# Optimization experiments

Measured on AMD Instinct MI355X. Metric: run time of the kernel, lower is better.

## Reference

```python
import jax, jax.numpy as jnp
import numpy as np

IOU_THRESH = 0.6
IMG_SIZE = 2048.0


def _iou_matrix(boxes):
    # boxes: [N, 4] as (x1, y1, x2, y2)
    x1, y1, x2, y2 = boxes[:, 0], boxes[:, 1], boxes[:, 2], boxes[:, 3]
    area = jnp.maximum(x2 - x1, 0.0) * jnp.maximum(y2 - y1, 0.0)  # [N]
    ix1 = jnp.maximum(x1[:, None], x1[None, :])
    iy1 = jnp.maximum(y1[:, None], y1[None, :])
    ix2 = jnp.minimum(x2[:, None], x2[None, :])
    iy2 = jnp.minimum(y2[:, None], y2[None, :])
    inter = jnp.maximum(ix2 - ix1, 0.0) * jnp.maximum(iy2 - iy1, 0.0)  # [N, N]
    union = area[:, None] + area[None, :] - inter
    return inter / jnp.maximum(union, 1e-9)


def _nms_keep(boxes, thresh):
    # Greedy NMS in the given (score-sorted) order; returns a [N] bool keep mask.
    n = boxes.shape[0]
    iou = _iou_matrix(boxes)  # [N, N] -- dominant memory traffic
    idx = jnp.arange(n)

    def step(suppressed, i):
        keep_i = jnp.logical_not(suppressed[i])
        # a kept box suppresses all LATER boxes with IoU > thresh
        suppressed = suppressed | (keep_i & (idx > i) & (iou[i] > thresh))
        return suppressed, keep_i

    _, keep = jax.lax.scan(step, jnp.zeros((n,), dtype=bool), idx)
    return keep


def _make_boxes(kc, ks, n):
    c = jax.random.uniform(kc, (n, 2), minval=0.0, maxval=IMG_SIZE)
    s = jax.random.uniform(ks, (n, 2), minval=10.0, maxval=120.0)
    return jnp.concatenate([c - s / 2, c + s / 2], axis=1)  # [n, 4]


def setup_inputs() -> dict:
    key = jax.random.key(0)
    k1, k2, k3, k4, k5, k6 = jax.random.split(key, 6)
    N = 8192  # vstacked detections across projections
    M = 8192  # vstacked RPN rois across projections
    det_boxes = _make_boxes(k1, k2, N)
    cls_scores = jax.random.normal(k3, (N, 4), dtype=jnp.float32)  # 4 TL classes, class 0 = invalid
    proj_id = jnp.zeros((N, 1), dtype=jnp.float32)
    detections = jnp.concatenate([proj_id, det_boxes, cls_scores], axis=1)  # [N, 9]
    rpn_boxes = _make_boxes(k4, k5, M)
    objness = jax.random.uniform(k6, (M, 1), dtype=jnp.float32)
    rpn_data = jnp.concatenate([jnp.zeros((M, 1), dtype=jnp.float32), rpn_boxes, objness], axis=1)  # [M, 6]
    return {"detections": detections, "rpn_data": rpn_data}


def reference(detections, rpn_data):
    # detect(): NMS(0.6) on detections[:, 1:5] and on rpn_data[:, 1:5]
    keep_det = _nms_keep(detections[:, 1:5], IOU_THRESH)  # [N] bool
    keep_rpn = _nms_keep(rpn_data[:, 1:5], IOU_THRESH)    # [M] bool
    # forward(): split surviving detections into valid (tl_type != 0) / invalid
    tl_types = jnp.argmax(detections[:, 5:], axis=1)
    valid_mask = keep_det & (tl_types != 0)
    invalid_mask = keep_det & (tl_types == 0)
    # fixed-shape (jit-friendly) masked outputs instead of data-dependent gather
    valid_detections = detections * valid_mask[:, None].astype(detections.dtype)
    invalid_detections = detections * invalid_mask[:, None].astype(detections.dtype)
    rpn_attack_data = rpn_data * keep_rpn[:, None].astype(rpn_data.dtype)
    return valid_detections, invalid_detections, rpn_attack_data
```

## Files before the change

kernel.cpp:

```cpp
#include <hip/hip_runtime.h>


constexpr int NROWS = 8192;
constexpr int NKW   = 256;
constexpr unsigned ACAP = 512;
constexpr unsigned BCAP = 1536;
constexpr unsigned RCAP = 2048;
constexpr unsigned ELDS = 16384;
#define IOU_T 0.6f

constexpr size_t OFF_ECNT  = 0;
constexpr size_t OFF_BCNT  = 2048;
constexpr size_t OFF_OVF   = 4096;
constexpr size_t OFF_EDGES = 8192;
constexpr size_t OFF_BBOX  = OFF_EDGES + (size_t)512 * RCAP * 4;
constexpr size_t OFF_BID   = OFF_BBOX  + (size_t)512 * ACAP * 16;

__global__ __launch_bounds__(512) void bin_kernel(
    const float* __restrict__ det, const float* __restrict__ rpn,
    unsigned* __restrict__ binCnt, float4* __restrict__ binBox,
    unsigned* __restrict__ binId, unsigned* __restrict__ ovf)
{
  const int b = blockIdx.x;
  const int set = b >> 4;
  const int r = ((b & 15) << 9) + threadIdx.x;
  const float* src  = (set == 0) ? det : rpn;
  const int    strd = (set == 0) ? 9 : 6;

  const float* p = src + (size_t)r * strd + 1;
  const float x1 = p[0], y1 = p[1], x2 = p[2], y2 = p[3];
  const float cxe = 0.5f * (x1 + x2), cye = 0.5f * (y1 + y2);
  const int ccx = min(15, max(0, (int)(cxe * (1.0f / 128.0f))));
  const int ccy = min(15, max(0, (int)(cye * (1.0f / 128.0f))));
  const unsigned cell = (unsigned)(set * 256 + ccy * 16 + ccx);

  const unsigned slot = atomicAdd(&binCnt[cell], 1u);
  if (slot < ACAP) {
    binBox[(size_t)cell * ACAP + slot] = make_float4(x1, y1, x2, y2);
    binId [(size_t)cell * ACAP + slot] = (unsigned)r;
  } else {
    atomicOr(ovf, 1u);
  }
}

__global__ __launch_bounds__(512) void pair_kernel(
    const float* __restrict__ det, const float* __restrict__ rpn,
    const unsigned* __restrict__ binCnt, const float4* __restrict__ binBox,
    const unsigned* __restrict__ binId, const unsigned* __restrict__ ovfp,
    unsigned* __restrict__ cnts, unsigned* __restrict__ edges)
{
  const int cellid = blockIdx.x, set = blockIdx.y;
  const int cx = cellid & 15, cy = cellid >> 4;
  unsigned* myedges = edges + ((size_t)(set * 256 + cellid)) * RCAP;

  __shared__ float4 B4[BCAP];
  __shared__ float  Bar[BCAP];
  __shared__ unsigned Bid[BCAP];
  __shared__ unsigned ncell[9], ncnt[9], noff[9];
  __shared__ unsigned nN_sh, na_sh, nb_sh, eCnt, bad;

  const int t = threadIdx.x;
  if (t == 0) {
    unsigned nN = 0;
    ncell[nN++] = (unsigned)(set * 256 + cellid);
    for (int dy = -1; dy <= 1; ++dy)
      for (int dx = -1; dx <= 1; ++dx) {
        if (dx == 0 && dy == 0) continue;
        const int nx = cx + dx, ny = cy + dy;
        if (nx >= 0 && nx < 16 && ny >= 0 && ny < 16)
          ncell[nN++] = (unsigned)(set * 256 + ny * 16 + nx);
      }
    nN_sh = nN; eCnt = 0u; bad = *ovfp;
  }
  __syncthreads();
  const unsigned nN = nN_sh;
  if (t < (int)nN) ncnt[t] = min(binCnt[ncell[t]], ACAP);
  __syncthreads();
  if (t == 0) {
    unsigned off = 0;
    for (unsigned n = 0; n < nN; ++n) { noff[n] = off; off += ncnt[n]; }
    na_sh = ncnt[0]; nb_sh = off;
    if (off > BCAP) bad = 1u;
  }
  __syncthreads();

  const unsigned na = na_sh, nb = nb_sh;
  const bool ok = (bad == 0u);

  if (ok) {
    for (unsigned idx = t; idx < nb; idx += 512) {
      unsigned n = 0;
      while (idx >= noff[n] + ncnt[n]) ++n;
      const unsigned k = idx - noff[n];
      const size_t  g = (size_t)ncell[n] * ACAP + k;
      const float4 bx = binBox[g];
      B4[idx]  = bx;
      Bar[idx] = fmaxf(bx.z - bx.x, 0.0f) * fmaxf(bx.w - bx.y, 0.0f);
      Bid[idx] = binId[g];
    }
  }
  __syncthreads();

  if (ok) {
    const unsigned tot = na * nb;
    for (unsigned p = t; p < tot; p += 512) {
      const unsigned ai = p / nb, x = p - ai * nb;
      const unsigned ia = Bid[ai], ib = Bid[x];
      if (ia < ib) {
        const float4 A = B4[ai], B = B4[x];
        const float ix1 = fmaxf(A.x, B.x), iy1 = fmaxf(A.y, B.y);
        const float ix2 = fminf(A.z, B.z), iy2 = fminf(A.w, B.w);
        const float inter = fmaxf(ix2 - ix1, 0.0f) * fmaxf(iy2 - iy1, 0.0f);
        if (inter > 0.0f) {
          const float uni = Bar[ai] + Bar[x] - inter;
          const float iou = inter / fmaxf(uni, 1e-9f);
          if (iou > IOU_T) {
            const unsigned slot = atomicAdd(&eCnt, 1u);
            if (slot < RCAP) myedges[slot] = (ia << 13) | ib;
          }
        }
      }
    }
  } else {
    const float* src  = (set == 0) ? det : rpn;
    const int    strd = (set == 0) ? 9 : 6;
    for (int ra = 0; ra < NROWS; ++ra) {
      const float* pa = src + (size_t)ra * strd + 1;
      const float ax1 = pa[0], ay1 = pa[1], ax2 = pa[2], ay2 = pa[3];
      const float cxe = 0.5f * (ax1 + ax2), cye = 0.5f * (ay1 + ay2);
      const int ccx = min(15, max(0, (int)(cxe * (1.0f / 128.0f))));
      const int ccy = min(15, max(0, (int)(cye * (1.0f / 128.0f))));
      if (ccx != cx || ccy != cy) continue;
      const float aar = fmaxf(ax2 - ax1, 0.0f) * fmaxf(ay2 - ay1, 0.0f);
      for (int rb = t; rb < NROWS; rb += 512) {
        if ((unsigned)ra >= (unsigned)rb) continue;
        const float* pb = src + (size_t)rb * strd + 1;
        const float bx1 = pb[0], by1 = pb[1], bx2 = pb[2], by2 = pb[3];
        const float ix1 = fmaxf(ax1, bx1), iy1 = fmaxf(ay1, by1);
        const float ix2 = fminf(ax2, bx2), iy2 = fminf(ay2, by2);
        const float inter = fmaxf(ix2 - ix1, 0.0f) * fmaxf(iy2 - iy1, 0.0f);
        if (inter > 0.0f) {
          const float bar = fmaxf(bx2 - bx1, 0.0f) * fmaxf(by2 - by1, 0.0f);
          const float uni = aar + bar - inter;
          const float iou = inter / fmaxf(uni, 1e-9f);
          if (iou > IOU_T) {
            const unsigned slot = atomicAdd(&eCnt, 1u);
            if (slot < RCAP) myedges[slot] = ((unsigned)ra << 13) | (unsigned)rb;
          }
        }
      }
    }
  }
  __syncthreads();
  if (t == 0) cnts[set * 256 + cellid] = min(eCnt, RCAP);
}

__global__ __launch_bounds__(1024) void solve_epi_kernel(
    const float* __restrict__ det, const float* __restrict__ rpn,
    const unsigned* __restrict__ cnts, const unsigned* __restrict__ edges,
    float* __restrict__ out)
{
  const int blk = blockIdx.x;
  const int set = blk >> 4;
  const int slice = blk & 15;
  const unsigned* gedges = edges + (size_t)set * 256 * RCAP;

  __shared__ unsigned eL[ELDS];
  __shared__ unsigned rcnt[256], roff[256];
  __shared__ unsigned kbuf[2][NKW];
  __shared__ int changed[2];
  __shared__ unsigned Etot_sh;
  __shared__ float vmsk[512], imsk[512];

  const int t = threadIdx.x;
  if (t < 256) rcnt[t] = min(cnts[set * 256 + t], RCAP);
  __syncthreads();

  if (t < 64) {
    const unsigned h0 = rcnt[4 * t], h1 = rcnt[4 * t + 1];
    const unsigned h2 = rcnt[4 * t + 2], h3 = rcnt[4 * t + 3];
    const unsigned lsum = h0 + h1 + h2 + h3;
    unsigned incl = lsum;
    #pragma unroll
    for (int d = 1; d < 64; d <<= 1) {
      const unsigned v = __shfl_up(incl, d);
      if (t >= d) incl += v;
    }
    const unsigned base = incl - lsum;
    roff[4 * t] = base;               roff[4 * t + 1] = base + h0;
    roff[4 * t + 2] = base + h0 + h1; roff[4 * t + 3] = base + h0 + h1 + h2;
    if (t == 63) Etot_sh = incl;
  }
  if (t < NKW) kbuf[0][t] = 0xFFFFFFFFu;
  __syncthreads();

  const unsigned Etot = Etot_sh;
  const bool cached = (Etot <= ELDS);
  if (cached) {
    const unsigned rg = (unsigned)t >> 2, ln = (unsigned)t & 3u;
    const unsigned c = rcnt[rg], o = roff[rg];
    for (unsigned k = ln; k < c; k += 4u)
      eL[o + k] = gedges[(size_t)rg * RCAP + k];
  }
  __syncthreads();

  int cur = 0;
  for (int round = 0; round < NROWS + 8; ++round) {
    const int nxt = cur ^ 1;
    if (t == 0) changed[round & 1] = 0;
    if (t < NKW) kbuf[nxt][t] = 0xFFFFFFFFu;
    __syncthreads();

    if (cached) {
      for (unsigned e = t; e < Etot; e += 1024) {
        const unsigned pk = eL[e];
        const unsigned i = pk >> 13, j = pk & 8191u;
        if ((kbuf[cur][i >> 5] >> (i & 31)) & 1u)
          atomicAnd(&kbuf[nxt][j >> 5], ~(1u << (j & 31)));
      }
    } else {
      for (unsigned r = (unsigned)t >> 2; r < 256u; r += 256u) {
        const unsigned c = rcnt[r];
        for (unsigned k = (unsigned)t & 3u; k < c; k += 4u) {
          const unsigned pk = gedges[(size_t)r * RCAP + k];
          const unsigned i = pk >> 13, j = pk & 8191u;
          if ((kbuf[cur][i >> 5] >> (i & 31)) & 1u)
            atomicAnd(&kbuf[nxt][j >> 5], ~(1u << (j & 31)));
        }
      }
    }
    __syncthreads();

    if (t < NKW && kbuf[nxt][t] != kbuf[cur][t]) changed[round & 1] = 1;
    __syncthreads();

    cur = nxt;
    if (!changed[round & 1]) break;
  }

  const int r0 = slice * 512;
  if (set == 0) {
    if (t < 512) {
      const int i = r0 + t;
      const bool kd = (kbuf[cur][i >> 5] >> (i & 31)) & 1u;
      const float* p = det + (size_t)i * 9;
      const float sc0 = p[5], sc1 = p[6], sc2 = p[7], sc3 = p[8];
      int am = 0; float best = sc0;
      if (sc1 > best) { best = sc1; am = 1; }
      if (sc2 > best) { best = sc2; am = 2; }
      if (sc3 > best) { best = sc3; am = 3; }
      vmsk[t] = (kd && am != 0) ? 1.0f : 0.0f;
      imsk[t] = (kd && am == 0) ? 1.0f : 0.0f;
    }
    __syncthreads();
    const float4* in4 = reinterpret_cast<const float4*>(det + (size_t)r0 * 9);
    float4* o0 = reinterpret_cast<float4*>(out + (size_t)r0 * 9);
    float4* o1 = reinterpret_cast<float4*>(out + (size_t)NROWS * 9 + (size_t)r0 * 9);
    for (int q = t; q < 1152; q += 1024) {
      const float4 v = in4[q];
      const float* vp = reinterpret_cast<const float*>(&v);
      float4 a, b;
      float* ap = reinterpret_cast<float*>(&a);
      float* bp = reinterpret_cast<float*>(&b);
      #pragma unroll
      for (int j = 0; j < 4; ++j) {
        const unsigned d = (unsigned)(q * 4 + j);
        const unsigned row = (d * 7282u) >> 16;
        ap[j] = vp[j] * vmsk[row];
        bp[j] = vp[j] * imsk[row];
      }
      o0[q] = a; o1[q] = b;
    }
  } else {
    if (t < 512) {
      const int i = r0 + t;
      const bool kr = (kbuf[cur][i >> 5] >> (i & 31)) & 1u;
      vmsk[t] = kr ? 1.0f : 0.0f;
    }
    __syncthreads();
    const float4* in4 = reinterpret_cast<const float4*>(rpn + (size_t)r0 * 6);
    float4* o2 = reinterpret_cast<float4*>(out + (size_t)NROWS * 18 + (size_t)r0 * 6);
    for (int q = t; q < 768; q += 1024) {
      const float4 v = in4[q];
      const float* vp = reinterpret_cast<const float*>(&v);
      float4 a;
      float* ap = reinterpret_cast<float*>(&a);
      #pragma unroll
      for (int j = 0; j < 4; ++j) {
        const unsigned d = (unsigned)(q * 4 + j);
        const unsigned row = (d * 10923u) >> 16;
        ap[j] = vp[j] * vmsk[row];
      }
      o2[q] = a;
    }
  }
}

extern "C" void kernel_launch(void* const* d_in, const int* in_sizes, int n_in,
                              void* d_out, int out_size, void* d_ws, size_t ws_size,
                              hipStream_t stream)
{
  const float* det = (const float*)d_in[0];
  const float* rpn = (const float*)d_in[1];
  float* out = (float*)d_out;

  char* ws = (char*)d_ws;
  unsigned* ecnt   = (unsigned*)(ws + OFF_ECNT);
  unsigned* binCnt = (unsigned*)(ws + OFF_BCNT);
  unsigned* ovf    = (unsigned*)(ws + OFF_OVF);
  unsigned* edges  = (unsigned*)(ws + OFF_EDGES);
  float4*   binBox = (float4*)  (ws + OFF_BBOX);
  unsigned* binId  = (unsigned*)(ws + OFF_BID);

  hipMemsetAsync(ws + OFF_BCNT, 0, 2048 + 64, stream);

  bin_kernel<<<32, 512, 0, stream>>>(det, rpn, binCnt, binBox, binId, ovf);

  dim3 g1(256, 2);
  pair_kernel<<<g1, 512, 0, stream>>>(det, rpn, binCnt, binBox, binId, ovf,
                                      ecnt, edges);

  solve_epi_kernel<<<32, 1024, 0, stream>>>(det, rpn, ecnt, edges, out);
}
```

Baseline: 79.49 us.

## Fuse bin, pair and solve stages into one cooperative kernel with grid syncs

Replaces the memset and three separate kernel launches with a single cooperative kernel of 512 blocks that zeroes the counters, bins boxes, builds IoU edges per cell and runs the iterative NMS solve, separated by grid.sync() barriers. Shared memory for the pair and solve phases is overlaid through a union. The solve phase drops from 1024 to 512 threads per block, and the LDS edge cache shrinks from 16384 to 12288 entries to fit the tighter occupancy target. The aim is to remove launch and memset overhead. In exchange it pays grid-barrier costs, leaves only 32 blocks active during the long solve loop, gives that loop half the threads, and falls back to global edge reads more often because the cache is smaller.

```diff
diff --git a/kernel.cpp b/kernel.cpp
--- a/kernel.cpp
+++ b/kernel.cpp
@@ -1,4 +1,7 @@
 #include <hip/hip_runtime.h>
+#include <hip/hip_cooperative_groups.h>
+
+namespace cg = cooperative_groups;
 
 
 constexpr int NROWS = 8192;
@@ -6,7 +9,7 @@
 constexpr unsigned ACAP = 512;
 constexpr unsigned BCAP = 1536;
 constexpr unsigned RCAP = 2048;
-constexpr unsigned ELDS = 16384;
+constexpr unsigned ELDS = 12288;
 #define IOU_T 0.6f
 
 constexpr size_t OFF_ECNT  = 0;
@@ -16,169 +19,178 @@
 constexpr size_t OFF_BBOX  = OFF_EDGES + (size_t)512 * RCAP * 4;
 constexpr size_t OFF_BID   = OFF_BBOX  + (size_t)512 * ACAP * 16;
 
-__global__ __launch_bounds__(512) void bin_kernel(
+union __align__(16) Smem {
+  struct {
+    float4   B4[BCAP];
+    float    Bar[BCAP];
+    unsigned Bid[BCAP];
+  } p;
+  struct {
+    unsigned eL[ELDS];
+    unsigned rcnt[256], roff[256];
+    unsigned kbuf[2][NKW];
+    float    vmsk[512], imsk[512];
+  } s;
+};
+
+__global__ __launch_bounds__(512, 4) void fused_kernel(
     const float* __restrict__ det, const float* __restrict__ rpn,
-    unsigned* __restrict__ binCnt, float4* __restrict__ binBox,
-    unsigned* __restrict__ binId, unsigned* __restrict__ ovf)
+    unsigned* __restrict__ ecnt, unsigned* __restrict__ binCnt,
+    unsigned* __restrict__ ovf,  unsigned* __restrict__ edges,
+    float4* __restrict__ binBox, unsigned* __restrict__ binId,
+    float* __restrict__ out)
 {
-  const int b = blockIdx.x;
-  const int set = b >> 4;
-  const int r = ((b & 15) << 9) + threadIdx.x;
-  const float* src  = (set == 0) ? det : rpn;
-  const int    strd = (set == 0) ? 9 : 6;
-
-  const float* p = src + (size_t)r * strd + 1;
-  const float x1 = p[0], y1 = p[1], x2 = p[2], y2 = p[3];
-  const float cxe = 0.5f * (x1 + x2), cye = 0.5f * (y1 + y2);
-  const int ccx = min(15, max(0, (int)(cxe * (1.0f / 128.0f))));
-  const int ccy = min(15, max(0, (int)(cye * (1.0f / 128.0f))));
-  const unsigned cell = (unsigned)(set * 256 + ccy * 16 + ccx);
-
-  const unsigned slot = atomicAdd(&binCnt[cell], 1u);
-  if (slot < ACAP) {
-    binBox[(size_t)cell * ACAP + slot] = make_float4(x1, y1, x2, y2);
-    binId [(size_t)cell * ACAP + slot] = (unsigned)r;
-  } else {
-    atomicOr(ovf, 1u);
-  }
-}
-
-__global__ __launch_bounds__(512) void pair_kernel(
-    const float* __restrict__ det, const float* __restrict__ rpn,
-    const unsigned* __restrict__ binCnt, const float4* __restrict__ binBox,
-    const unsigned* __restrict__ binId, const unsigned* __restrict__ ovfp,
-    unsigned* __restrict__ cnts, unsigned* __restrict__ edges)
-{
-  const int cellid = blockIdx.x, set = blockIdx.y;
-  const int cx = cellid & 15, cy = cellid >> 4;
-  unsigned* myedges = edges + ((size_t)(set * 256 + cellid)) * RCAP;
-
-  __shared__ float4 B4[BCAP];
-  __shared__ float  Bar[BCAP];
-  __shared__ unsigned Bid[BCAP];
-  __shared__ unsigned ncell[9], ncnt[9], noff[9];
-  __shared__ unsigned nN_sh, na_sh, nb_sh, eCnt, bad;
-
-  const int t = threadIdx.x;
-  if (t == 0) {
-    unsigned nN = 0;
-    ncell[nN++] = (unsigned)(set * 256 + cellid);
-    for (int dy = -1; dy <= 1; ++dy)
-      for (int dx = -1; dx <= 1; ++dx) {
-        if (dx == 0 && dy == 0) continue;
-        const int nx = cx + dx, ny = cy + dy;
-        if (nx >= 0 && nx < 16 && ny >= 0 && ny < 16)
-          ncell[nN++] = (unsigned)(set * 256 + ny * 16 + nx);
-      }
-    nN_sh = nN; eCnt = 0u; bad = *ovfp;
-  }
-  __syncthreads();
-  const unsigned nN = nN_sh;
-  if (t < (int)nN) ncnt[t] = min(binCnt[ncell[t]], ACAP);
-  __syncthreads();
-  if (t == 0) {
-    unsigned off = 0;
-    for (unsigned n = 0; n < nN; ++n) { noff[n] = off; off += ncnt[n]; }
-    na_sh = ncnt[0]; nb_sh = off;
-    if (off > BCAP) bad = 1u;
-  }
-  __syncthreads();
-
-  const unsigned na = na_sh, nb = nb_sh;
-  const bool ok = (bad == 0u);
-
-  if (ok) {
-    for (unsigned idx = t; idx < nb; idx += 512) {
-      unsigned n = 0;
-      while (idx >= noff[n] + ncnt[n]) ++n;
-      const unsigned k = idx - noff[n];
-      const size_t  g = (size_t)ncell[n] * ACAP + k;
-      const float4 bx = binBox[g];
-      B4[idx]  = bx;
-      Bar[idx] = fmaxf(bx.z - bx.x, 0.0f) * fmaxf(bx.w - bx.y, 0.0f);
-      Bid[idx] = binId[g];
-    }
-  }
-  __syncthreads();
-
-  if (ok) {
-    const unsigned tot = na * nb;
-    for (unsigned p = t; p < tot; p += 512) {
-      const unsigned ai = p / nb, x = p - ai * nb;
-      const unsigned ia = Bid[ai], ib = Bid[x];
-      if (ia < ib) {
-        const float4 A = B4[ai], B = B4[x];
-        const float ix1 = fmaxf(A.x, B.x), iy1 = fmaxf(A.y, B.y);
-        const float ix2 = fminf(A.z, B.z), iy2 = fminf(A.w, B.w);
-        const float inter = fmaxf(ix2 - ix1, 0.0f) * fmaxf(iy2 - iy1, 0.0f);
-        if (inter > 0.0f) {
-          const float uni = Bar[ai] + Bar[x] - inter;
-          const float iou = inter / fmaxf(uni, 1e-9f);
-          if (iou > IOU_T) {
-            const unsigned slot = atomicAdd(&eCnt, 1u);
-            if (slot < RCAP) myedges[slot] = (ia << 13) | ib;
+  cg::grid_group grid = cg::this_grid();
+  __shared__ Smem U;
+  __shared__ unsigned ncell[9], ncnt9[9], noff9[9];
+  __shared__ unsigned nN_sh, na_sh, nb_sh, eC, bad;
+  __shared__ unsigned Etot_sh;
+  __shared__ int changed[2];
+
+  const int bid = blockIdx.x;
+  const int t   = threadIdx.x;
+
+  if (bid == 0) { binCnt[t] = 0u; if (t == 0) *ovf = 0u; }
+  grid.sync();
+
+  {
+    const int gtid = (bid << 9) + t;
+    if (gtid < 2 * NROWS) {
+      const int bset = gtid >> 13;
+      const int r    = gtid & (NROWS - 1);
+      const float* src  = (bset == 0) ? det : rpn;
+      const int    strd = (bset == 0) ? 9 : 6;
+      const float* p = src + (size_t)r * strd + 1;
+      const float x1 = p[0], y1 = p[1], x2 = p[2], y2 = p[3];
+      const float cxe = 0.5f * (x1 + x2), cye = 0.5f * (y1 + y2);
+      const int ccx = min(15, max(0, (int)(cxe * (1.0f / 128.0f))));
+      const int ccy = min(15, max(0, (int)(cye * (1.0f / 128.0f))));
+      const unsigned cell = (unsigned)(bset * 256 + ccy * 16 + ccx);
+      const unsigned slot = atomicAdd(&binCnt[cell], 1u);
+      if (slot < ACAP) {
+        binBox[(size_t)cell * ACAP + slot] = make_float4(x1, y1, x2, y2);
+        binId [(size_t)cell * ACAP + slot] = (unsigned)r;
+      } else {
+        atomicOr(ovf, 1u);
+      }
+    }
+  }
+  grid.sync();
+
+  {
+    const int set = bid >> 8;
+    const int cellid = bid & 255;
+    const int cx = cellid & 15, cy = cellid >> 4;
+    unsigned* myedges = edges + ((size_t)(set * 256 + cellid)) * RCAP;
+
+    if (t == 0) {
+      unsigned nN = 0;
+      ncell[nN++] = (unsigned)(set * 256 + cellid);
+      for (int dy = -1; dy <= 1; ++dy)
+        for (int dx = -1; dx <= 1; ++dx) {
+          if (dx == 0 && dy == 0) continue;
+          const int nx = cx + dx, ny = cy + dy;
+          if (nx >= 0 && nx < 16 && ny >= 0 && ny < 16)
+            ncell[nN++] = (unsigned)(set * 256 + ny * 16 + nx);
+        }
+      nN_sh = nN; eC = 0u; bad = *ovf;
+    }
+    __syncthreads();
+    const unsigned nN = nN_sh;
+    if (t < (int)nN) ncnt9[t] = min(binCnt[ncell[t]], ACAP);
+    __syncthreads();
+    if (t == 0) {
+      unsigned off = 0;
+      for (unsigned n = 0; n < nN; ++n) { noff9[n] = off; off += ncnt9[n]; }
+      na_sh = ncnt9[0]; nb_sh = off;
+      if (off > BCAP) bad = 1u;
+    }
+    __syncthreads();
+
+    const unsigned na = na_sh, nb = nb_sh;
+    const bool ok = (bad == 0u);
+
+    if (ok) {
+      for (unsigned idx = t; idx < nb; idx += 512) {
+        unsigned n = 0;
+        while (idx >= noff9[n] + ncnt9[n]) ++n;
+        const unsigned k = idx - noff9[n];
+        const size_t  g = (size_t)ncell[n] * ACAP + k;
+        const float4 bx = binBox[g];
+        U.p.B4[idx]  = bx;
+        U.p.Bar[idx] = fmaxf(bx.z - bx.x, 0.0f) * fmaxf(bx.w - bx.y, 0.0f);
+        U.p.Bid[idx] = binId[g];
+      }
+    }
+    __syncthreads();
+
+    if (ok) {
+      const unsigned tot = na * nb;
+      for (unsigned pi = t; pi < tot; pi += 512) {
+        const unsigned ai = pi / nb, x = pi - ai * nb;
+        const unsigned ia = U.p.Bid[ai], ib = U.p.Bid[x];
+        if (ia < ib) {
+          const float4 A = U.p.B4[ai], B = U.p.B4[x];
+          const float ix1 = fmaxf(A.x, B.x), iy1 = fmaxf(A.y, B.y);
+          const float ix2 = fminf(A.z, B.z), iy2 = fminf(A.w, B.w);
+          const float inter = fmaxf(ix2 - ix1, 0.0f) * fmaxf(iy2 - iy1, 0.0f);
+          if (inter > 0.0f) {
+            const float uni = U.p.Bar[ai] + U.p.Bar[x] - inter;
+            const float iou = inter / fmaxf(uni, 1e-9f);
+            if (iou > IOU_T) {
+              const unsigned slot = atomicAdd(&eC, 1u);
+              if (slot < RCAP) myedges[slot] = (ia << 13) | ib;
+            }
           }
         }
       }
-    }
-  } else {
-    const float* src  = (set == 0) ? det : rpn;
-    const int    strd = (set == 0) ? 9 : 6;
-    for (int ra = 0; ra < NROWS; ++ra) {
-      const float* pa = src + (size_t)ra * strd + 1;
-      const float ax1 = pa[0], ay1 = pa[1], ax2 = pa[2], ay2 = pa[3];
-      const float cxe = 0.5f * (ax1 + ax2), cye = 0.5f * (ay1 + ay2);
-      const int ccx = min(15, max(0, (int)(cxe * (1.0f / 128.0f))));
-      const int ccy = min(15, max(0, (int)(cye * (1.0f / 128.0f))));
-      if (ccx != cx || ccy != cy) continue;
-      const float aar = fmaxf(ax2 - ax1, 0.0f) * fmaxf(ay2 - ay1, 0.0f);
-      for (int rb = t; rb < NROWS; rb += 512) {
-        if ((unsigned)ra >= (unsigned)rb) continue;
-        const float* pb = src + (size_t)rb * strd + 1;
-        const float bx1 = pb[0], by1 = pb[1], bx2 = pb[2], by2 = pb[3];
-        const float ix1 = fmaxf(ax1, bx1), iy1 = fmaxf(ay1, by1);
-        const float ix2 = fminf(ax2, bx2), iy2 = fminf(ay2, by2);
-        const float inter = fmaxf(ix2 - ix1, 0.0f) * fmaxf(iy2 - iy1, 0.0f);
-        if (inter > 0.0f) {
-          const float bar = fmaxf(bx2 - bx1, 0.0f) * fmaxf(by2 - by1, 0.0f);
-          const float uni = aar + bar - inter;
-          const float iou = inter / fmaxf(uni, 1e-9f);
-          if (iou > IOU_T) {
-            const unsigned slot = atomicAdd(&eCnt, 1u);
-            if (slot < RCAP) myedges[slot] = ((unsigned)ra << 13) | (unsigned)rb;
+    } else {
+      const float* src  = (set == 0) ? det : rpn;
+      const int    strd = (set == 0) ? 9 : 6;
+      for (int ra = 0; ra < NROWS; ++ra) {
+        const float* pa = src + (size_t)ra * strd + 1;
+        const float ax1 = pa[0], ay1 = pa[1], ax2 = pa[2], ay2 = pa[3];
+        const float cxe = 0.5f * (ax1 + ax2), cye = 0.5f * (ay1 + ay2);
+        const int ccx = min(15, max(0, (int)(cxe * (1.0f / 128.0f))));
+        const int ccy = min(15, max(0, (int)(cye * (1.0f / 128.0f))));
+        if (ccx != cx || ccy != cy) continue;
+        const float aar = fmaxf(ax2 - ax1, 0.0f) * fmaxf(ay2 - ay1, 0.0f);
+        for (int rb = t; rb < NROWS; rb += 512) {
+          if ((unsigned)ra >= (unsigned)rb) continue;
+          const float* pb = src + (size_t)rb * strd + 1;
+          const float bx1 = pb[0], by1 = pb[1], bx2 = pb[2], by2 = pb[3];
+          const float ix1 = fmaxf(ax1, bx1), iy1 = fmaxf(ay1, by1);
+          const float ix2 = fminf(ax2, bx2), iy2 = fminf(ay2, by2);
+          const float inter = fmaxf(ix2 - ix1, 0.0f) * fmaxf(iy2 - iy1, 0.0f);
+          if (inter > 0.0f) {
+            const float bar = fmaxf(bx2 - bx1, 0.0f) * fmaxf(by2 - by1, 0.0f);
+            const float uni = aar + bar - inter;
+            const float iou = inter / fmaxf(uni, 1e-9f);
+            if (iou > IOU_T) {
+              const unsigned slot = atomicAdd(&eC, 1u);
+              if (slot < RCAP) myedges[slot] = ((unsigned)ra << 13) | (unsigned)rb;
+            }
           }
         }
       }
     }
-  }
+    __syncthreads();
+    if (t == 0) ecnt[set * 256 + cellid] = min(eC, RCAP);
+  }
+  grid.sync();
+
+  if (bid >= 32) return;
+
+  const int set = bid >> 4;
+  const int slice = bid & 15;
+  const unsigned* gedges = edges + (size_t)set * 256 * RCAP;
+
+  if (t < 256) U.s.rcnt[t] = min(ecnt[set * 256 + t], RCAP);
   __syncthreads();
-  if (t == 0) cnts[set * 256 + cellid] = min(eCnt, RCAP);
-}
-
-__global__ __launch_bounds__(1024) void solve_epi_kernel(
-    const float* __restrict__ det, const float* __restrict__ rpn,
-    const unsigned* __restrict__ cnts, const unsigned* __restrict__ edges,
-    float* __restrict__ out)
-{
-  const int blk = blockIdx.x;
-  const int set = blk >> 4;
-  const int slice = blk & 15;
-  const unsigned* gedges = edges + (size_t)set * 256 * RCAP;
-
-  __shared__ unsigned eL[ELDS];
-  __shared__ unsigned rcnt[256], roff[256];
-  __shared__ unsigned kbuf[2][NKW];
-  __shared__ int changed[2];
-  __shared__ unsigned Etot_sh;
-  __shared__ float vmsk[512], imsk[512];
-
-  const int t = threadIdx.x;
-  if (t < 256) rcnt[t] = min(cnts[set * 256 + t], RCAP);
-  __syncthreads();
 
   if (t < 64) {
-    const unsigned h0 = rcnt[4 * t], h1 = rcnt[4 * t + 1];
-    const unsigned h2 = rcnt[4 * t + 2], h3 = rcnt[4 * t + 3];
+    const unsigned h0 = U.s.rcnt[4 * t], h1 = U.s.rcnt[4 * t + 1];
+    const unsigned h2 = U.s.rcnt[4 * t + 2], h3 = U.s.rcnt[4 * t + 3];
     const unsigned lsum = h0 + h1 + h2 + h3;
     unsigned incl = lsum;
     #pragma unroll
@@ -187,20 +199,20 @@
       if (t >= d) incl += v;
     }
     const unsigned base = incl - lsum;
-    roff[4 * t] = base;               roff[4 * t + 1] = base + h0;
-    roff[4 * t + 2] = base + h0 + h1; roff[4 * t + 3] = base + h0 + h1 + h2;
+    U.s.roff[4 * t] = base;                     U.s.roff[4 * t + 1] = base + h0;
+    U.s.roff[4 * t + 2] = base + h0 + h1;       U.s.roff[4 * t + 3] = base + h0 + h1 + h2;
     if (t == 63) Etot_sh = incl;
   }
-  if (t < NKW) kbuf[0][t] = 0xFFFFFFFFu;
+  if (t < NKW) U.s.kbuf[0][t] = 0xFFFFFFFFu;
   __syncthreads();
 
   const unsigned Etot = Etot_sh;
   const bool cached = (Etot <= ELDS);
   if (cached) {
-    const unsigned rg = (unsigned)t >> 2, ln = (unsigned)t & 3u;
-    const unsigned c = rcnt[rg], o = roff[rg];
-    for (unsigned k = ln; k < c; k += 4u)
-      eL[o + k] = gedges[(size_t)rg * RCAP + k];
+    const unsigned rg = (unsigned)t >> 1, ln = (unsigned)t & 1u;
+    const unsigned c = U.s.rcnt[rg], o = U.s.roff[rg];
+    for (unsigned k = ln; k < c; k += 2u)
+      U.s.eL[o + k] = gedges[(size_t)rg * RCAP + k];
   }
   __syncthreads();
 
@@ -208,30 +220,30 @@
   for (int round = 0; round < NROWS + 8; ++round) {
     const int nxt = cur ^ 1;
     if (t == 0) changed[round & 1] = 0;
-    if (t < NKW) kbuf[nxt][t] = 0xFFFFFFFFu;
+    if (t < NKW) U.s.kbuf[nxt][t] = 0xFFFFFFFFu;
     __syncthreads();
 
     if (cached) {
-      for (unsigned e = t; e < Etot; e += 1024) {
-        const unsigned pk = eL[e];
+      for (unsigned e = t; e < Etot; e += 512) {
+        const unsigned pk = U.s.eL[e];
         const unsigned i = pk >> 13, j = pk & 8191u;
-        if ((kbuf[cur][i >> 5] >> (i & 31)) & 1u)
-          atomicAnd(&kbuf[nxt][j >> 5], ~(1u << (j & 31)));
+        if ((U.s.kbuf[cur][i >> 5] >> (i & 31)) & 1u)
+          atomicAnd(&U.s.kbuf[nxt][j >> 5], ~(1u << (j & 31)));
       }
     } else {
-      for (unsigned r = (unsigned)t >> 2; r < 256u; r += 256u) {
-        const unsigned c = rcnt[r];
-        for (unsigned k = (unsigned)t & 3u; k < c; k += 4u) {
+      for (unsigned r = (unsigned)t >> 1; r < 256u; r += 256u) {
+        const unsigned c = U.s.rcnt[r];
+        for (unsigned k = (unsigned)t & 1u; k < c; k += 2u) {
           const unsigned pk = gedges[(size_t)r * RCAP + k];
           const unsigned i = pk >> 13, j = pk & 8191u;
-          if ((kbuf[cur][i >> 5] >> (i & 31)) & 1u)
-            atomicAnd(&kbuf[nxt][j >> 5], ~(1u << (j & 31)));
+          if ((U.s.kbuf[cur][i >> 5] >> (i & 31)) & 1u)
+            atomicAnd(&U.s.kbuf[nxt][j >> 5], ~(1u << (j & 31)));
         }
       }
     }
     __syncthreads();
 
-    if (t < NKW && kbuf[nxt][t] != kbuf[cur][t]) changed[round & 1] = 1;
+    if (t < NKW && U.s.kbuf[nxt][t] != U.s.kbuf[cur][t]) changed[round & 1] = 1;
     __syncthreads();
 
     cur = nxt;
@@ -240,23 +252,23 @@
 
   const int r0 = slice * 512;
   if (set == 0) {
-    if (t < 512) {
+    {
       const int i = r0 + t;
-      const bool kd = (kbuf[cur][i >> 5] >> (i & 31)) & 1u;
+      const bool kd = (U.s.kbuf[cur][i >> 5] >> (i & 31)) & 1u;
       const float* p = det + (size_t)i * 9;
       const float sc0 = p[5], sc1 = p[6], sc2 = p[7], sc3 = p[8];
       int am = 0; float best = sc0;
       if (sc1 > best) { best = sc1; am = 1; }
       if (sc2 > best) { best = sc2; am = 2; }
       if (sc3 > best) { best = sc3; am = 3; }
-      vmsk[t] = (kd && am != 0) ? 1.0f : 0.0f;
-      imsk[t] = (kd && am == 0) ? 1.0f : 0.0f;
+      U.s.vmsk[t] = (kd && am != 0) ? 1.0f : 0.0f;
+      U.s.imsk[t] = (kd && am == 0) ? 1.0f : 0.0f;
     }
     __syncthreads();
     const float4* in4 = reinterpret_cast<const float4*>(det + (size_t)r0 * 9);
     float4* o0 = reinterpret_cast<float4*>(out + (size_t)r0 * 9);
     float4* o1 = reinterpret_cast<float4*>(out + (size_t)NROWS * 9 + (size_t)r0 * 9);
-    for (int q = t; q < 1152; q += 1024) {
+    for (int q = t; q < 1152; q += 512) {
       const float4 v = in4[q];
       const float* vp = reinterpret_cast<const float*>(&v);
       float4 a, b;
@@ -266,21 +278,21 @@
       for (int j = 0; j < 4; ++j) {
         const unsigned d = (unsigned)(q * 4 + j);
         const unsigned row = (d * 7282u) >> 16;
-        ap[j] = vp[j] * vmsk[row];
-        bp[j] = vp[j] * imsk[row];
+        ap[j] = vp[j] * U.s.vmsk[row];
+        bp[j] = vp[j] * U.s.imsk[row];
       }
       o0[q] = a; o1[q] = b;
     }
   } else {
-    if (t < 512) {
+    {
       const int i = r0 + t;
-      const bool kr = (kbuf[cur][i >> 5] >> (i & 31)) & 1u;
-      vmsk[t] = kr ? 1.0f : 0.0f;
+      const bool kr = (U.s.kbuf[cur][i >> 5] >> (i & 31)) & 1u;
+      U.s.vmsk[t] = kr ? 1.0f : 0.0f;
     }
     __syncthreads();
     const float4* in4 = reinterpret_cast<const float4*>(rpn + (size_t)r0 * 6);
     float4* o2 = reinterpret_cast<float4*>(out + (size_t)NROWS * 18 + (size_t)r0 * 6);
-    for (int q = t; q < 768; q += 1024) {
+    for (int q = t; q < 768; q += 512) {
       const float4 v = in4[q];
       const float* vp = reinterpret_cast<const float*>(&v);
       float4 a;
@@ -289,7 +301,7 @@
       for (int j = 0; j < 4; ++j) {
         const unsigned d = (unsigned)(q * 4 + j);
         const unsigned row = (d * 10923u) >> 16;
-        ap[j] = vp[j] * vmsk[row];
+        ap[j] = vp[j] * U.s.vmsk[row];
       }
       o2[q] = a;
     }
@@ -312,13 +324,9 @@
   float4*   binBox = (float4*)  (ws + OFF_BBOX);
   unsigned* binId  = (unsigned*)(ws + OFF_BID);
 
-  hipMemsetAsync(ws + OFF_BCNT, 0, 2048 + 64, stream);
-
-  bin_kernel<<<32, 512, 0, stream>>>(det, rpn, binCnt, binBox, binId, ovf);
-
-  dim3 g1(256, 2);
-  pair_kernel<<<g1, 512, 0, stream>>>(det, rpn, binCnt, binBox, binId, ovf,
-                                      ecnt, edges);
-
-  solve_epi_kernel<<<32, 1024, 0, stream>>>(det, rpn, ecnt, edges, out);
+  void* args[] = { (void*)&det, (void*)&rpn, (void*)&ecnt, (void*)&binCnt,
+                   (void*)&ovf, (void*)&edges, (void*)&binBox, (void*)&binId,
+                   (void*)&out };
+  hipLaunchCooperativeKernel((const void*)fused_kernel, dim3(512), dim3(512),
+                             args, 0, stream);
 }
```

Result: slower. 218.9 us (+175.4%).
